# Performance work log

Measured on AMD Instinct MI355X. Metric: run time of the kernel, lower is better.

The kernel has to match this reference:

```python
import jax, jax.numpy as jnp
import numpy as np

# Clebsch-Gordan coefficients in the real basis; l=1 components stored in (y,z,x) order
S2 = 1.0 / np.sqrt(2.0)
S3 = 1.0 / np.sqrt(3.0)
S6 = 1.0 / np.sqrt(6.0)
_C2 = np.zeros((5, 3, 3), np.float32)
_C2[0, 2, 0] = _C2[0, 0, 2] = S2          # ~ xy
_C2[1, 0, 1] = _C2[1, 1, 0] = S2          # ~ yz
_C2[2, 1, 1] = 2.0 * S6                   # ~ 2z^2 - x^2 - y^2
_C2[2, 2, 2] = -S6
_C2[2, 0, 0] = -S6
_C2[3, 2, 1] = _C2[3, 1, 2] = S2          # ~ xz
_C2[4, 2, 2] = S2                          # ~ x^2 - y^2
_C2[4, 0, 0] = -S2
C2 = jnp.asarray(_C2)

N0, N1 = 64, 32        # multiplicities of input 0e / 1o irreps
CUTOFF = 5.0


def basis_functions(pos):
    """pos [N,3] -> (scalars [N,64], l=1 features [N,32,3])."""
    r = jnp.linalg.norm(pos, axis=-1, keepdims=True) + 1e-9        # [N,1]
    d = pos[:, (1, 2, 0)] / r                                       # unit dir, (y,z,x) order
    c0 = jnp.linspace(0.0, CUTOFF, N0, dtype=pos.dtype)
    c1 = jnp.linspace(0.0, CUTOFF, N1, dtype=pos.dtype)
    f0 = jnp.exp(-4.0 * (r - c0) ** 2)                              # [N,64] gaussian RBF
    f1 = jnp.exp(-4.0 * (r - c1) ** 2)                              # [N,32]
    x1 = f1[:, :, None] * d[:, None, :]                             # [N,32,3]
    return f0, x1


def lin_l(x, W):
    # channel mixing within one irrep block; preserves the m axis if present
    if x.ndim == 2:
        return x @ W
    return jnp.einsum('ncm,cd->ndm', x, W)


def tensor_product(a0, a1, b0, b1):
    """Full uvw CG tensor product of (64x0 + 32x1) x (64x0 + 32x1)."""
    N = a0.shape[0]
    # l=0 outputs: 0x0->0 and 1x1->0
    p000 = jnp.einsum('na,nb->nab', a0, b0).reshape(N, -1)                 # [N,4096]
    p110 = jnp.einsum('nam,nbm->nab', a1, b1).reshape(N, -1) * S3          # [N,1024]
    t0 = jnp.concatenate([p000, p110], axis=1)                             # [N,5120]
    # l=1 outputs: 0x1->1, 1x0->1, 1x1->1 (cross product)
    p011 = (a0[:, :, None, None] * b1[:, None, :, :]).reshape(N, -1, 3)    # [N,2048,3]
    p101 = (a1[:, :, None, :] * b0[:, None, :, None]).reshape(N, -1, 3)    # [N,2048,3]
    p111 = (jnp.cross(a1[:, :, None, :], b1[:, None, :, :]) * S2).reshape(N, -1, 3)
    t1 = jnp.concatenate([p011, p101, p111], axis=1)                       # [N,5120,3]
    # l=2 output: 1x1->2 via CG tensor
    t2 = jnp.einsum('nai,nbj,mij->nabm', a1, b1, C2).reshape(N, -1, 5)     # [N,1024,5]
    return t0, t1, t2


def setup_inputs() -> dict:
    key = jax.random.key(0)
    ks = jax.random.split(key, 10)
    N = 4096
    def w(k, i, o):
        return jax.random.normal(k, (i, o), jnp.float32) / np.sqrt(i)
    return {
        'positions': jax.random.normal(ks[0], (N, 3), jnp.float32) * 2.0,
        'W1_0': w(ks[1], 64, 64),
        'W1_1': w(ks[2], 32, 32),
        'W2_0': w(ks[3], 64, 64),
        'W2_1': w(ks[4], 32, 32),
        'W3_0': w(ks[5], 5120, 64),
        'W3_1': w(ks[6], 5120, 32),
        'W3_2': w(ks[7], 1024, 16),
        'W_out': w(ks[8], 240, 7),
        'b_out': jnp.zeros((7,), jnp.float32),
    }


def reference(positions, W1_0, W1_1, W2_0, W2_1, W3_0, W3_1, W3_2, W_out, b_out):
    f0, f1 = basis_functions(positions)                 # 64x0, 32x1
    a0, a1 = lin_l(f0, W1_0), lin_l(f1, W1_1)           # linear1
    b0, b1 = lin_l(f0, W2_0), lin_l(f1, W2_1)           # linear2
    t0, t1, t2 = tensor_product(a0, a1, b0, b1)         # 5120x0, 5120x1, 1024x2
    y0 = lin_l(t0, W3_0)                                # [N,64]
    y1 = lin_l(t1, W3_1)                                # [N,32,3]
    y2 = lin_l(t2, W3_2)                                # [N,16,5]
    N = y0.shape[0]
    feat = jnp.concatenate([y0, y1.reshape(N, -1), y2.reshape(N, -1)], axis=1)  # [N,240]
    return feat @ W_out + b_out                         # [N,7]
```

## Files before the change

### kernel.cpp

```cpp
#include <hip/hip_runtime.h>
#include <math.h>

#define NS2 0.70710678118654752440f
#define NS3 0.57735026918962576451f
#define NS6 0.40824829046386301636f

typedef _Float16 f16;
typedef _Float16 f16x8 __attribute__((ext_vector_type(8)));
typedef float    f32x4 __attribute__((ext_vector_type(4)));

#define GT_K    22528
#define UV_ROW  216
#define OFF_UV  157696

__device__ __forceinline__ void build_gt(
    const float* __restrict__ W3_0, const float* __restrict__ W3_1,
    const float* __restrict__ W3_2, const float* __restrict__ Wout,
    f16* __restrict__ wsh, float* smem, int k_base, int n_k)
{
    const int tid = threadIdx.x;
    float* s_wo  = smem;
    float* s_red = smem + 1680;
    for (int i = tid; i < 1680; i += 256) s_wo[i] = Wout[i];
    __syncthreads();
    const int kl = tid & 63, q = tid >> 6;
    if (kl < n_k) {
        const int k = k_base + kl;
        float acc[7] = {0.f,0.f,0.f,0.f,0.f,0.f,0.f};
        if (k < 4096) {
            const float* wr = W3_0 + (size_t)k * 64;
            #pragma unroll
            for (int oo = 0; oo < 16; oo += 4) {
                int o = q*16 + oo;
                float4 wv = *(const float4*)(wr + o);
                const float* w0 = s_wo + o * 7;
                #pragma unroll
                for (int kk = 0; kk < 7; ++kk)
                    acc[kk] = fmaf(wv.x, w0[kk], fmaf(wv.y, w0[7+kk],
                              fmaf(wv.z, w0[14+kk], fmaf(wv.w, w0[21+kk], acc[kk]))));
            }
        } else if (k < 10240) {
            int it = k >> 6, s = it - 64, m = s >> 5, a2 = s & 31, l = k & 63;
            const float* wr = W3_1 + (size_t)(2048 + a2*64 + l) * 32;
            #pragma unroll
            for (int oo = 0; oo < 8; oo += 4) {
                int o = q*8 + oo;
                float4 wv = *(const float4*)(wr + o);
                const float* w0 = s_wo + (64 + o*3 + m) * 7;
                #pragma unroll
                for (int kk = 0; kk < 7; ++kk)
                    acc[kk] = fmaf(wv.x, w0[kk], fmaf(wv.y, w0[21+kk],
                              fmaf(wv.z, w0[42+kk], fmaf(wv.w, w0[63+kk], acc[kk]))));
            }
        } else {
            int it2 = (k - 10240) >> 5, l32 = k & 31;
            if (it2 < 32) {
                const float* wr = W3_0 + (size_t)(4096 + it2*32 + l32) * 64;
                #pragma unroll
                for (int oo = 0; oo < 16; oo += 4) {
                    int o = q*16 + oo;
                    float4 wv = *(const float4*)(wr + o);
                    const float* w0 = s_wo + o * 7;
                    #pragma unroll
                    for (int kk = 0; kk < 7; ++kk)
                        acc[kk] = fmaf(wv.x, w0[kk], fmaf(wv.y, w0[7+kk],
                                  fmaf(wv.z, w0[14+kk], fmaf(wv.w, w0[21+kk], acc[kk]))));
                }
            } else if (it2 < 224) {
                int t = it2 - 32, m = t >> 6, a = t & 63;
                const float* wr = W3_1 + (size_t)(a*32 + l32) * 32;
                #pragma unroll
                for (int oo = 0; oo < 8; oo += 4) {
                    int o = q*8 + oo;
                    float4 wv = *(const float4*)(wr + o);
                    const float* w0 = s_wo + (64 + o*3 + m) * 7;
                    #pragma unroll
                    for (int kk = 0; kk < 7; ++kk)
                        acc[kk] = fmaf(wv.x, w0[kk], fmaf(wv.y, w0[21+kk],
                                  fmaf(wv.z, w0[42+kk], fmaf(wv.w, w0[63+kk], acc[kk]))));
                }
            } else {
                int t = it2 - 224, m = t >> 5, a = t & 31;
                const float* wr = W3_2 + (size_t)(a*32 + l32) * 16;
                int o = q*4;
                float4 wv = *(const float4*)(wr + o);
                const float* w0 = s_wo + (160 + o*5 + m) * 7;
                #pragma unroll
                for (int kk = 0; kk < 7; ++kk)
                    acc[kk] = fmaf(wv.x, w0[kk], fmaf(wv.y, w0[35+kk],
                              fmaf(wv.z, w0[70+kk], fmaf(wv.w, w0[105+kk], acc[kk]))));
            }
        }
        #pragma unroll
        for (int r = 0; r < 7; ++r) s_red[(q*64 + kl)*8 + r] = acc[r];
    }
    __syncthreads();
    if (tid < n_k) {
        #pragma unroll
        for (int r = 0; r < 7; ++r) {
            float v = s_red[(      tid)*8 + r] + s_red[( 64 + tid)*8 + r]
                    + s_red[(128 + tid)*8 + r] + s_red[(192 + tid)*8 + r];
            wsh[(size_t)r * GT_K + k_base + tid] = (f16)v;
        }
    }
}

__device__ __forceinline__ void build_nodes(
    const float* __restrict__ pos,
    const float* __restrict__ W1_0, const float* __restrict__ W1_1,
    const float* __restrict__ W2_0, const float* __restrict__ W2_1,
    const float* __restrict__ bout,
    f16* __restrict__ wsh, float* __restrict__ out, float* smem, int base)
{
    const int tid = threadIdx.x;
    float* s_f0 = smem;
    float* s_f1 = smem + 512;
    f16* uv = wsh + OFF_UV;
    {
        int d = tid & 63;
        #pragma unroll
        for (int jj = 0; jj < 2; ++jj) {
            int j = (tid >> 6) + jj * 4;
            int n = base + j;
            float px = pos[n*3+0], py = pos[n*3+1], pz = pos[n*3+2];
            float r  = sqrtf(px*px + py*py + pz*pz) + 1e-9f;
            float t0 = r - (5.0f/63.0f) * (float)d;
            s_f0[j*64 + d] = __expf(-4.f * t0 * t0);
        }
        {
            int j = tid >> 5, d1 = tid & 31;
            int n = base + j;
            float px = pos[n*3+0], py = pos[n*3+1], pz = pos[n*3+2];
            float r  = sqrtf(px*px + py*py + pz*pz) + 1e-9f;
            float t1 = r - (5.0f/31.0f) * (float)d1;
            s_f1[j*32 + d1] = __expf(-4.f * t1 * t1);
        }
        if (tid < 8) {
            int n = base + tid;
            float px = pos[n*3+0], py = pos[n*3+1], pz = pos[n*3+2];
            float r  = sqrtf(px*px + py*py + pz*pz) + 1e-9f;
            float iv = 1.0f / r;
            float d0 = py*iv, d1 = pz*iv, d2 = px*iv;
            f16* row = uv + (size_t)n * UV_ROW;
            row[192+0] = (f16)d0;
            row[192+1] = (f16)d1;
            row[192+2] = (f16)d2;
            row[192+3] = (f16)(NS3 * (d0*d0 + d1*d1 + d2*d2));
            row[192+4] = (f16)(2.f*NS2*d2*d0);
            row[192+5] = (f16)(2.f*NS2*d0*d1);
            row[192+6] = (f16)(NS6*(2.f*d1*d1 - d2*d2 - d0*d0));
            row[192+7] = (f16)(2.f*NS2*d2*d1);
            row[192+8] = (f16)(NS2*(d2*d2 - d0*d0));
            row[201]   = (f16)1.0f;
        }
        if (tid < 56) out[base*7 + tid] = bout[tid % 7];
    }
    __syncthreads();
    {
        int c = tid & 63, jb = tid >> 6;
        float aa0 = 0.f, aa1 = 0.f, ba0 = 0.f, ba1 = 0.f;
        const float* wa = W1_0 + c;
        const float* wb = W2_0 + c;
        #pragma unroll 4
        for (int d = 0; d < 64; ++d) {
            float wav = wa[d*64], wbv = wb[d*64];
            float fA = s_f0[jb*64 + d], fB = s_f0[(jb+4)*64 + d];
            aa0 = fmaf(fA, wav, aa0);  aa1 = fmaf(fB, wav, aa1);
            ba0 = fmaf(fA, wbv, ba0);  ba1 = fmaf(fB, wbv, ba1);
        }
        uv[(size_t)(base+jb  )*UV_ROW +      c] = (f16)aa0;
        uv[(size_t)(base+jb+4)*UV_ROW +      c] = (f16)aa1;
        uv[(size_t)(base+jb  )*UV_ROW + 96 + c] = (f16)ba0;
        uv[(size_t)(base+jb+4)*UV_ROW + 96 + c] = (f16)ba1;

        int c1 = tid & 31, j8 = tid >> 5;
        float aA = 0.f, aB = 0.f;
        const float* wA = W1_1 + c1;
        const float* wB = W2_1 + c1;
        #pragma unroll 4
        for (int d = 0; d < 32; ++d) {
            float f = s_f1[j8*32 + d];
            aA = fmaf(f, wA[d*32], aA);
            aB = fmaf(f, wB[d*32], aB);
        }
        uv[(size_t)(base+j8)*UV_ROW +  64 + c1] = (f16)aA;
        uv[(size_t)(base+j8)*UV_ROW + 160 + c1] = (f16)aB;
    }
}

__global__ __launch_bounds__(256) void prep_kernel(
    const float* __restrict__ pos,
    const float* __restrict__ W1_0, const float* __restrict__ W1_1,
    const float* __restrict__ W2_0, const float* __restrict__ W2_1,
    const float* __restrict__ W3_0, const float* __restrict__ W3_1,
    const float* __restrict__ W3_2, const float* __restrict__ Wout,
    const float* __restrict__ bout,
    f16* __restrict__ wsh, float* __restrict__ out, int N)
{
    __shared__ __align__(16) float smem[3728];
    (void)N;
    build_gt(W3_0, W3_1, W3_2, Wout, wsh, smem, blockIdx.x * 44, 44);
    build_nodes(pos, W1_0, W1_1, W2_0, W2_1, bout, wsh, out, smem,
                blockIdx.x * 8);
}

__global__ __launch_bounds__(256) void main_kernel(
    const f16* __restrict__ wsh, float* __restrict__ out, int N)
{
    __shared__ __align__(16) char smem[79248];
    f16* s_g   = (f16*)smem;
    f16* s_uv  = (f16*)(smem + 39648);
    f16* s_ugt = (f16*)(smem + 67296);
    unsigned short* s_idx = (unsigned short*)(smem + 79072);
    (void)N;

    const int tid  = threadIdx.x;
    const int w    = tid >> 6;
    const int lane = tid & 63;
    const int lq   = lane >> 4;
    const int lm   = lane & 15;
    const int ra   = lm % 7;
    const int g    = blockIdx.x >> 3;
    const int kq   = blockIdx.x & 7;

    uint4 ru[7];
    {
        const uint4* src = (const uint4*)(wsh + OFF_UV + (size_t)g * 64 * UV_ROW);
        #pragma unroll
        for (int it = 0; it < 7; ++it) {
            int j = tid + it*256;
            if (j < 1728) ru[it] = src[j];
        }
    }
    uint4 rg[10];
    #pragma unroll
    for (int it = 0; it < 10; ++it) {
        int j = tid + it*256;
        if (j < 2464) {
            int row = j / 352, col = j - row*352;
            size_t off = (size_t)row * GT_K +
                         (col < 160 ? kq*1280 + col*8
                                    : 10240 + kq*1536 + (col-160)*8);
            rg[it] = *(const uint4*)(wsh + off);
        }
    }
    if (tid < 88) {
        int c  = tid;
        int gc = (c < 40) ? (kq*40 + c) : (320 + kq*48 + (c - 40));
        int uidx, gidx;
        if (gc < 320) {
            int it = gc >> 1;
            if (it < 64) { uidx = it; gidx = 9; }
            else { int s = it - 64; uidx = 64 + (s & 31); gidx = s >> 5; }
        } else {
            int it2 = gc - 320;
            if (it2 < 32)       { uidx = 64 + it2;                  gidx = 3; }
            else if (it2 < 224) { int t = it2 - 32;  uidx = t & 63;         gidx = t >> 6; }
            else                { int t = it2 - 224; uidx = 64 + (t & 31);  gidx = 4 + (t >> 5); }
        }
        s_idx[c] = (unsigned short)(uidx | (gidx << 8));
    }
    {
        uint4* dst = (uint4*)s_uv;
        #pragma unroll
        for (int it = 0; it < 7; ++it) {
            int j = tid + it*256;
            if (j < 1728) dst[j] = ru[it];
        }
    }
    #pragma unroll
    for (int it = 0; it < 10; ++it) {
        int j = tid + it*256;
        if (j < 2464) {
            int row = j / 352, col = j - row*352;
            *(uint4*)(s_g + row*2832 + col*8) = rg[it];
        }
    }
    __syncthreads();

    #pragma unroll
    for (int it = 0; it < 22; ++it) {
        int j = tid + it*256;
        int n = j / 88, c = j - n*88;
        unsigned short ix = s_idx[c];
        float u  = (float)s_uv[n*UV_ROW + (ix & 255)];
        float gg = (float)s_uv[n*UV_ROW + 192 + (ix >> 8)];
        s_ugt[n*92 + c] = (f16)(u * gg);
    }
    const f16* myrow = s_uv + (w*16 + lm) * UV_ROW;
    f16x8 vA0 = *(const f16x8*)(myrow +  96 + lq*8);
    f16x8 vA1 = *(const f16x8*)(myrow + 128 + lq*8);
    f16x8 vB  = *(const f16x8*)(myrow + 160 + lq*8);
    __syncthreads();

    f32x4 acc0 = {0.f,0.f,0.f,0.f}, acc1 = {0.f,0.f,0.f,0.f};
    const f16* arow  = s_g + ra*2832 + lq*8;
    const f16* ugrow = s_ugt + (w*16 + lm)*92;
    #pragma unroll
    for (int cb = 0; cb < 5; ++cb) {
        f16x8 ug8 = *(const f16x8*)(ugrow + cb*8);
        #pragma unroll
        for (int s = 0; s < 8; ++s) {
            int c = cb*8 + s;
            f16x8 a  = *(const f16x8*)(arow + c*32);
            f16x8 vv = (s & 1) ? vA1 : vA0;
            f16 ug   = ug8[s];
            f16x8 b;
            #pragma unroll
            for (int j2 = 0; j2 < 8; ++j2) b[j2] = vv[j2] * ug;
            if (s & 1) acc1 = __builtin_amdgcn_mfma_f32_16x16x32_f16(a, b, acc1, 0, 0, 0);
            else       acc0 = __builtin_amdgcn_mfma_f32_16x16x32_f16(a, b, acc0, 0, 0, 0);
        }
    }
    #pragma unroll
    for (int cb = 5; cb < 11; ++cb) {
        f16x8 ug8 = *(const f16x8*)(ugrow + cb*8);
        #pragma unroll
        for (int s = 0; s < 8; ++s) {
            int c = cb*8 + s;
            f16x8 a  = *(const f16x8*)(arow + c*32);
            f16 ug   = ug8[s];
            f16x8 b;
            #pragma unroll
            for (int j2 = 0; j2 < 8; ++j2) b[j2] = vB[j2] * ug;
            if (s & 1) acc1 = __builtin_amdgcn_mfma_f32_16x16x32_f16(a, b, acc1, 0, 0, 0);
            else       acc0 = __builtin_amdgcn_mfma_f32_16x16x32_f16(a, b, acc0, 0, 0, 0);
        }
    }

    int node = g*64 + w*16 + lm;
    if (lq == 0) {
        #pragma unroll
        for (int r = 0; r < 4; ++r) atomicAdd(&out[node*7 + r], acc0[r] + acc1[r]);
    } else if (lq == 1) {
        #pragma unroll
        for (int r = 0; r < 3; ++r) atomicAdd(&out[node*7 + 4 + r], acc0[r] + acc1[r]);
    }
}

extern "C" void kernel_launch(void* const* d_in, const int* in_sizes, int n_in,
                              void* d_out, int out_size, void* d_ws, size_t ws_size,
                              hipStream_t stream)
{
    const float* pos  = (const float*)d_in[0];
    const float* W1_0 = (const float*)d_in[1];
    const float* W1_1 = (const float*)d_in[2];
    const float* W2_0 = (const float*)d_in[3];
    const float* W2_1 = (const float*)d_in[4];
    const float* W3_0 = (const float*)d_in[5];
    const float* W3_1 = (const float*)d_in[6];
    const float* W3_2 = (const float*)d_in[7];
    const float* Wout = (const float*)d_in[8];
    const float* bout = (const float*)d_in[9];
    f16*   wsh = (f16*)d_ws;
    float* op  = (float*)d_out;
    int N = in_sizes[0] / 3;

    prep_kernel<<<512, 256, 0, stream>>>(pos, W1_0, W1_1, W2_0, W2_1,
                                         W3_0, W3_1, W3_2, Wout, bout, wsh, op, N);
    main_kernel<<<512, 256, 0, stream>>>(wsh, op, N);
}
```

Baseline: 104.8 us.

## Move node features into main kernel and double-buffer weight slices over K

Per-node feature construction (RBF, linear1/2, direction harmonics) moves from the prep kernel into the main kernel, so node data stays in shared memory instead of going through global workspace. Each main block now owns 16 nodes and loops over all 8 K-slices of the folded weight matrix. The next slice is loaded into a double buffer while the current one is computed, with K split across waves. Per-wave partial sums are reduced in shared memory and written once with the bias, replacing atomicAdd. The trade-off is fewer blocks (256), roughly 93 KB of shared memory per block with one block per CU, and the weights being re-read by every block.

```diff
diff --git a/kernel.cpp b/kernel.cpp
--- a/kernel.cpp
+++ b/kernel.cpp
@@ -9,26 +9,51 @@
 typedef _Float16 f16x8 __attribute__((ext_vector_type(8)));
 typedef float    f32x4 __attribute__((ext_vector_type(4)));
 
-#define GT_K    22528
-#define UV_ROW  216
-#define OFF_UV  157696
-
-__device__ __forceinline__ void build_gt(
+#define EI 19712
+
+__global__ __launch_bounds__(256) void prep_kernel(
     const float* __restrict__ W3_0, const float* __restrict__ W3_1,
     const float* __restrict__ W3_2, const float* __restrict__ Wout,
-    f16* __restrict__ wsh, float* smem, int k_base, int n_k)
+    f16* __restrict__ wsh)
 {
-    const int tid = threadIdx.x;
+    __shared__ __align__(16) float smem[3728];
     float* s_wo  = smem;
     float* s_red = smem + 1680;
+    const int tid = threadIdx.x;
     for (int i = tid; i < 1680; i += 256) s_wo[i] = Wout[i];
     __syncthreads();
     const int kl = tid & 63, q = tid >> 6;
-    if (kl < n_k) {
-        const int k = k_base + kl;
-        float acc[7] = {0.f,0.f,0.f,0.f,0.f,0.f,0.f};
-        if (k < 4096) {
-            const float* wr = W3_0 + (size_t)k * 64;
+    const int k  = blockIdx.x * 64 + kl;
+    float acc[7] = {0.f,0.f,0.f,0.f,0.f,0.f,0.f};
+    if (k < 4096) {
+        const float* wr = W3_0 + (size_t)k * 64;
+        #pragma unroll
+        for (int oo = 0; oo < 16; oo += 4) {
+            int o = q*16 + oo;
+            float4 wv = *(const float4*)(wr + o);
+            const float* w0 = s_wo + o * 7;
+            #pragma unroll
+            for (int kk = 0; kk < 7; ++kk)
+                acc[kk] = fmaf(wv.x, w0[kk], fmaf(wv.y, w0[7+kk],
+                          fmaf(wv.z, w0[14+kk], fmaf(wv.w, w0[21+kk], acc[kk]))));
+        }
+    } else if (k < 10240) {
+        int it = k >> 6, s = it - 64, m = s >> 5, a2 = s & 31, l = k & 63;
+        const float* wr = W3_1 + (size_t)(2048 + a2*64 + l) * 32;
+        #pragma unroll
+        for (int oo = 0; oo < 8; oo += 4) {
+            int o = q*8 + oo;
+            float4 wv = *(const float4*)(wr + o);
+            const float* w0 = s_wo + (64 + o*3 + m) * 7;
+            #pragma unroll
+            for (int kk = 0; kk < 7; ++kk)
+                acc[kk] = fmaf(wv.x, w0[kk], fmaf(wv.y, w0[21+kk],
+                          fmaf(wv.z, w0[42+kk], fmaf(wv.w, w0[63+kk], acc[kk]))));
+        }
+    } else {
+        int it2 = (k - 10240) >> 5, l32 = k & 31;
+        if (it2 < 32) {
+            const float* wr = W3_0 + (size_t)(4096 + it2*32 + l32) * 64;
             #pragma unroll
             for (int oo = 0; oo < 16; oo += 4) {
                 int o = q*16 + oo;
@@ -39,9 +64,9 @@
                     acc[kk] = fmaf(wv.x, w0[kk], fmaf(wv.y, w0[7+kk],
                               fmaf(wv.z, w0[14+kk], fmaf(wv.w, w0[21+kk], acc[kk]))));
             }
-        } else if (k < 10240) {
-            int it = k >> 6, s = it - 64, m = s >> 5, a2 = s & 31, l = k & 63;
-            const float* wr = W3_1 + (size_t)(2048 + a2*64 + l) * 32;
+        } else if (it2 < 224) {
+            int t = it2 - 32, m = t >> 6, a = t & 63;
+            const float* wr = W3_1 + (size_t)(a*32 + l32) * 32;
             #pragma unroll
             for (int oo = 0; oo < 8; oo += 4) {
                 int o = q*8 + oo;
@@ -53,288 +78,250 @@
                               fmaf(wv.z, w0[42+kk], fmaf(wv.w, w0[63+kk], acc[kk]))));
             }
         } else {
-            int it2 = (k - 10240) >> 5, l32 = k & 31;
-            if (it2 < 32) {
-                const float* wr = W3_0 + (size_t)(4096 + it2*32 + l32) * 64;
-                #pragma unroll
-                for (int oo = 0; oo < 16; oo += 4) {
-                    int o = q*16 + oo;
-                    float4 wv = *(const float4*)(wr + o);
-                    const float* w0 = s_wo + o * 7;
-                    #pragma unroll
-                    for (int kk = 0; kk < 7; ++kk)
-                        acc[kk] = fmaf(wv.x, w0[kk], fmaf(wv.y, w0[7+kk],
-                                  fmaf(wv.z, w0[14+kk], fmaf(wv.w, w0[21+kk], acc[kk]))));
-                }
-            } else if (it2 < 224) {
-                int t = it2 - 32, m = t >> 6, a = t & 63;
-                const float* wr = W3_1 + (size_t)(a*32 + l32) * 32;
-                #pragma unroll
-                for (int oo = 0; oo < 8; oo += 4) {
-                    int o = q*8 + oo;
-                    float4 wv = *(const float4*)(wr + o);
-                    const float* w0 = s_wo + (64 + o*3 + m) * 7;
-                    #pragma unroll
-                    for (int kk = 0; kk < 7; ++kk)
-                        acc[kk] = fmaf(wv.x, w0[kk], fmaf(wv.y, w0[21+kk],
-                                  fmaf(wv.z, w0[42+kk], fmaf(wv.w, w0[63+kk], acc[kk]))));
-                }
-            } else {
-                int t = it2 - 224, m = t >> 5, a = t & 31;
-                const float* wr = W3_2 + (size_t)(a*32 + l32) * 16;
-                int o = q*4;
-                float4 wv = *(const float4*)(wr + o);
-                const float* w0 = s_wo + (160 + o*5 + m) * 7;
-                #pragma unroll
-                for (int kk = 0; kk < 7; ++kk)
-                    acc[kk] = fmaf(wv.x, w0[kk], fmaf(wv.y, w0[35+kk],
-                              fmaf(wv.z, w0[70+kk], fmaf(wv.w, w0[105+kk], acc[kk]))));
-            }
-        }
-        #pragma unroll
-        for (int r = 0; r < 7; ++r) s_red[(q*64 + kl)*8 + r] = acc[r];
-    }
-    __syncthreads();
-    if (tid < n_k) {
+            int t = it2 - 224, m = t >> 5, a = t & 31;
+            const float* wr = W3_2 + (size_t)(a*32 + l32) * 16;
+            int o = q*4;
+            float4 wv = *(const float4*)(wr + o);
+            const float* w0 = s_wo + (160 + o*5 + m) * 7;
+            #pragma unroll
+            for (int kk = 0; kk < 7; ++kk)
+                acc[kk] = fmaf(wv.x, w0[kk], fmaf(wv.y, w0[35+kk],
+                          fmaf(wv.z, w0[70+kk], fmaf(wv.w, w0[105+kk], acc[kk]))));
+        }
+    }
+    #pragma unroll
+    for (int r = 0; r < 7; ++r) s_red[(q*64 + kl)*8 + r] = acc[r];
+    __syncthreads();
+    if (tid < 64) {
+        int kk2 = blockIdx.x * 64 + tid;
+        int e, j;
+        if (kk2 < 10240) { e = kk2 / 1280; j = kk2 - e*1280; }
+        else { int kb = kk2 - 10240; e = kb / 1536; j = 1280 + kb - e*1536; }
+        f16* dst = wsh + e*EI + j;
         #pragma unroll
         for (int r = 0; r < 7; ++r) {
             float v = s_red[(      tid)*8 + r] + s_red[( 64 + tid)*8 + r]
                     + s_red[(128 + tid)*8 + r] + s_red[(192 + tid)*8 + r];
-            wsh[(size_t)r * GT_K + k_base + tid] = (f16)v;
+            dst[r*2816] = (f16)v;
         }
     }
 }
 
-__device__ __forceinline__ void build_nodes(
+__global__ __launch_bounds__(256, 1) void main_kernel(
+    const f16* __restrict__ wsh,
     const float* __restrict__ pos,
     const float* __restrict__ W1_0, const float* __restrict__ W1_1,
     const float* __restrict__ W2_0, const float* __restrict__ W2_1,
     const float* __restrict__ bout,
-    f16* __restrict__ wsh, float* __restrict__ out, float* smem, int base)
+    float* __restrict__ out, int N)
 {
-    const int tid = threadIdx.x;
-    float* s_f0 = smem;
-    float* s_f1 = smem + 512;
-    f16* uv = wsh + OFF_UV;
+    __shared__ __align__(16) char smem[93248];
+    f16* s_g   = (f16*)smem;
+    f16* s_uv  = (f16*)(smem + 79296);
+    f16* s_ugt = (f16*)(smem + 86208);
+    unsigned short* s_idx = (unsigned short*)(smem + 91840);
+    float* s_f0 = (float*)smem;
+    float* s_f1 = (float*)(smem + 4096);
+    (void)N;
+
+    const int tid  = threadIdx.x;
+    const int base = blockIdx.x * 16;
+
     {
         int d = tid & 63;
         #pragma unroll
-        for (int jj = 0; jj < 2; ++jj) {
-            int j = (tid >> 6) + jj * 4;
-            int n = base + j;
-            float px = pos[n*3+0], py = pos[n*3+1], pz = pos[n*3+2];
+        for (int it = 0; it < 4; ++it) {
+            int n = (tid >> 6) + it*4;
+            const float* pp = pos + (size_t)(base + n) * 3;
+            float px = pp[0], py = pp[1], pz = pp[2];
             float r  = sqrtf(px*px + py*py + pz*pz) + 1e-9f;
             float t0 = r - (5.0f/63.0f) * (float)d;
-            s_f0[j*64 + d] = __expf(-4.f * t0 * t0);
-        }
-        {
-            int j = tid >> 5, d1 = tid & 31;
-            int n = base + j;
-            float px = pos[n*3+0], py = pos[n*3+1], pz = pos[n*3+2];
+            s_f0[n*64 + d] = __expf(-4.f * t0 * t0);
+        }
+        int d1 = tid & 31;
+        #pragma unroll
+        for (int it = 0; it < 2; ++it) {
+            int n = (tid >> 5) + it*8;
+            const float* pp = pos + (size_t)(base + n) * 3;
+            float px = pp[0], py = pp[1], pz = pp[2];
             float r  = sqrtf(px*px + py*py + pz*pz) + 1e-9f;
             float t1 = r - (5.0f/31.0f) * (float)d1;
-            s_f1[j*32 + d1] = __expf(-4.f * t1 * t1);
-        }
-        if (tid < 8) {
-            int n = base + tid;
-            float px = pos[n*3+0], py = pos[n*3+1], pz = pos[n*3+2];
+            s_f1[n*32 + d1] = __expf(-4.f * t1 * t1);
+        }
+        if (tid < 16) {
+            const float* pp = pos + (size_t)(base + tid) * 3;
+            float px = pp[0], py = pp[1], pz = pp[2];
             float r  = sqrtf(px*px + py*py + pz*pz) + 1e-9f;
             float iv = 1.0f / r;
-            float d0 = py*iv, d1 = pz*iv, d2 = px*iv;
-            f16* row = uv + (size_t)n * UV_ROW;
+            float d0 = py*iv, dz = pz*iv, dx = px*iv;
+            f16* row = s_uv + tid*216;
             row[192+0] = (f16)d0;
-            row[192+1] = (f16)d1;
-            row[192+2] = (f16)d2;
-            row[192+3] = (f16)(NS3 * (d0*d0 + d1*d1 + d2*d2));
-            row[192+4] = (f16)(2.f*NS2*d2*d0);
-            row[192+5] = (f16)(2.f*NS2*d0*d1);
-            row[192+6] = (f16)(NS6*(2.f*d1*d1 - d2*d2 - d0*d0));
-            row[192+7] = (f16)(2.f*NS2*d2*d1);
-            row[192+8] = (f16)(NS2*(d2*d2 - d0*d0));
+            row[192+1] = (f16)dz;
+            row[192+2] = (f16)dx;
+            row[192+3] = (f16)(NS3 * (d0*d0 + dz*dz + dx*dx));
+            row[192+4] = (f16)(2.f*NS2*dx*d0);
+            row[192+5] = (f16)(2.f*NS2*d0*dz);
+            row[192+6] = (f16)(NS6*(2.f*dz*dz - dx*dx - d0*d0));
+            row[192+7] = (f16)(2.f*NS2*dx*dz);
+            row[192+8] = (f16)(NS2*(dx*dx - d0*d0));
             row[201]   = (f16)1.0f;
         }
-        if (tid < 56) out[base*7 + tid] = bout[tid % 7];
-    }
-    __syncthreads();
+        for (int c = tid; c < 704; c += 256) {
+            int p  = c / 88, cl = c - p*88;
+            int gc = (cl < 40) ? p*40 + cl : 320 + p*48 + (cl - 40);
+            int uidx, gidx;
+            if (gc < 320) {
+                int it = gc >> 1;
+                if (it < 64) { uidx = it; gidx = 9; }
+                else { int s = it - 64; uidx = 64 + (s & 31); gidx = s >> 5; }
+            } else {
+                int it2 = gc - 320;
+                if (it2 < 32)       { uidx = 64 + it2;                  gidx = 3; }
+                else if (it2 < 224) { int t = it2 - 32;  uidx = t & 63;         gidx = t >> 6; }
+                else                { int t = it2 - 224; uidx = 64 + (t & 31);  gidx = 4 + (t >> 5); }
+            }
+            s_idx[c] = (unsigned short)(uidx | (gidx << 8));
+        }
+    }
+    __syncthreads();
+
     {
         int c = tid & 63, jb = tid >> 6;
-        float aa0 = 0.f, aa1 = 0.f, ba0 = 0.f, ba1 = 0.f;
+        float a0a[4] = {0,0,0,0}, b0a[4] = {0,0,0,0};
         const float* wa = W1_0 + c;
         const float* wb = W2_0 + c;
-        #pragma unroll 4
         for (int d = 0; d < 64; ++d) {
             float wav = wa[d*64], wbv = wb[d*64];
-            float fA = s_f0[jb*64 + d], fB = s_f0[(jb+4)*64 + d];
-            aa0 = fmaf(fA, wav, aa0);  aa1 = fmaf(fB, wav, aa1);
-            ba0 = fmaf(fA, wbv, ba0);  ba1 = fmaf(fB, wbv, ba1);
-        }
-        uv[(size_t)(base+jb  )*UV_ROW +      c] = (f16)aa0;
-        uv[(size_t)(base+jb+4)*UV_ROW +      c] = (f16)aa1;
-        uv[(size_t)(base+jb  )*UV_ROW + 96 + c] = (f16)ba0;
-        uv[(size_t)(base+jb+4)*UV_ROW + 96 + c] = (f16)ba1;
-
+            #pragma unroll
+            for (int m = 0; m < 4; ++m) {
+                float f = s_f0[(jb + 4*m)*64 + d];
+                a0a[m] = fmaf(f, wav, a0a[m]);
+                b0a[m] = fmaf(f, wbv, b0a[m]);
+            }
+        }
+        #pragma unroll
+        for (int m = 0; m < 4; ++m) {
+            s_uv[(jb + 4*m)*216 +      c] = (f16)a0a[m];
+            s_uv[(jb + 4*m)*216 + 96 + c] = (f16)b0a[m];
+        }
         int c1 = tid & 31, j8 = tid >> 5;
-        float aA = 0.f, aB = 0.f;
+        float Aa[2] = {0,0}, Ba[2] = {0,0};
         const float* wA = W1_1 + c1;
         const float* wB = W2_1 + c1;
-        #pragma unroll 4
         for (int d = 0; d < 32; ++d) {
-            float f = s_f1[j8*32 + d];
-            aA = fmaf(f, wA[d*32], aA);
-            aB = fmaf(f, wB[d*32], aB);
-        }
-        uv[(size_t)(base+j8)*UV_ROW +  64 + c1] = (f16)aA;
-        uv[(size_t)(base+j8)*UV_ROW + 160 + c1] = (f16)aB;
-    }
-}
-
-__global__ __launch_bounds__(256) void prep_kernel(
-    const float* __restrict__ pos,
-    const float* __restrict__ W1_0, const float* __restrict__ W1_1,
-    const float* __restrict__ W2_0, const float* __restrict__ W2_1,
-    const float* __restrict__ W3_0, const float* __restrict__ W3_1,
-    const float* __restrict__ W3_2, const float* __restrict__ Wout,
-    const float* __restrict__ bout,
-    f16* __restrict__ wsh, float* __restrict__ out, int N)
-{
-    __shared__ __align__(16) float smem[3728];
-    (void)N;
-    build_gt(W3_0, W3_1, W3_2, Wout, wsh, smem, blockIdx.x * 44, 44);
-    build_nodes(pos, W1_0, W1_1, W2_0, W2_1, bout, wsh, out, smem,
-                blockIdx.x * 8);
-}
-
-__global__ __launch_bounds__(256) void main_kernel(
-    const f16* __restrict__ wsh, float* __restrict__ out, int N)
-{
-    __shared__ __align__(16) char smem[79248];
-    f16* s_g   = (f16*)smem;
-    f16* s_uv  = (f16*)(smem + 39648);
-    f16* s_ugt = (f16*)(smem + 67296);
-    unsigned short* s_idx = (unsigned short*)(smem + 79072);
-    (void)N;
-
-    const int tid  = threadIdx.x;
+            float wAv = wA[d*32], wBv = wB[d*32];
+            #pragma unroll
+            for (int m = 0; m < 2; ++m) {
+                float f = s_f1[(j8 + 8*m)*32 + d];
+                Aa[m] = fmaf(f, wAv, Aa[m]);
+                Ba[m] = fmaf(f, wBv, Ba[m]);
+            }
+        }
+        #pragma unroll
+        for (int m = 0; m < 2; ++m) {
+            s_uv[(j8 + 8*m)*216 +  64 + c1] = (f16)Aa[m];
+            s_uv[(j8 + 8*m)*216 + 160 + c1] = (f16)Ba[m];
+        }
+    }
+    __syncthreads();
+
     const int w    = tid >> 6;
     const int lane = tid & 63;
     const int lq   = lane >> 4;
     const int lm   = lane & 15;
     const int ra   = lm % 7;
-    const int g    = blockIdx.x >> 3;
-    const int kq   = blockIdx.x & 7;
-
-    uint4 ru[7];
-    {
-        const uint4* src = (const uint4*)(wsh + OFF_UV + (size_t)g * 64 * UV_ROW);
-        #pragma unroll
-        for (int it = 0; it < 7; ++it) {
-            int j = tid + it*256;
-            if (j < 1728) ru[it] = src[j];
-        }
-    }
-    uint4 rg[10];
-    #pragma unroll
-    for (int it = 0; it < 10; ++it) {
-        int j = tid + it*256;
-        if (j < 2464) {
-            int row = j / 352, col = j - row*352;
-            size_t off = (size_t)row * GT_K +
-                         (col < 160 ? kq*1280 + col*8
-                                    : 10240 + kq*1536 + (col-160)*8);
-            rg[it] = *(const uint4*)(wsh + off);
-        }
-    }
-    if (tid < 88) {
-        int c  = tid;
-        int gc = (c < 40) ? (kq*40 + c) : (320 + kq*48 + (c - 40));
-        int uidx, gidx;
-        if (gc < 320) {
-            int it = gc >> 1;
-            if (it < 64) { uidx = it; gidx = 9; }
-            else { int s = it - 64; uidx = 64 + (s & 31); gidx = s >> 5; }
-        } else {
-            int it2 = gc - 320;
-            if (it2 < 32)       { uidx = 64 + it2;                  gidx = 3; }
-            else if (it2 < 224) { int t = it2 - 32;  uidx = t & 63;         gidx = t >> 6; }
-            else                { int t = it2 - 224; uidx = 64 + (t & 31);  gidx = 4 + (t >> 5); }
-        }
-        s_idx[c] = (unsigned short)(uidx | (gidx << 8));
-    }
-    {
-        uint4* dst = (uint4*)s_uv;
-        #pragma unroll
-        for (int it = 0; it < 7; ++it) {
-            int j = tid + it*256;
-            if (j < 1728) dst[j] = ru[it];
-        }
-    }
-    #pragma unroll
-    for (int it = 0; it < 10; ++it) {
-        int j = tid + it*256;
-        if (j < 2464) {
-            int row = j / 352, col = j - row*352;
-            *(uint4*)(s_g + row*2832 + col*8) = rg[it];
-        }
-    }
-    __syncthreads();
-
-    #pragma unroll
-    for (int it = 0; it < 22; ++it) {
-        int j = tid + it*256;
-        int n = j / 88, c = j - n*88;
-        unsigned short ix = s_idx[c];
-        float u  = (float)s_uv[n*UV_ROW + (ix & 255)];
-        float gg = (float)s_uv[n*UV_ROW + 192 + (ix >> 8)];
-        s_ugt[n*92 + c] = (f16)(u * gg);
-    }
-    const f16* myrow = s_uv + (w*16 + lm) * UV_ROW;
+    const f16* myrow = s_uv + lm*216;
     f16x8 vA0 = *(const f16x8*)(myrow +  96 + lq*8);
     f16x8 vA1 = *(const f16x8*)(myrow + 128 + lq*8);
     f16x8 vB  = *(const f16x8*)(myrow + 160 + lq*8);
-    __syncthreads();
+
+    uint4 rg[10];
+    auto stage_load = [&](int p) {
+        const uint4* src = (const uint4*)(wsh + p*EI);
+        #pragma unroll
+        for (int it = 0; it < 10; ++it) {
+            int j = tid + it*256;
+            if (j < 2464) rg[it] = src[j];
+        }
+    };
+    auto stage_write = [&](int buf) {
+        f16* dst0 = s_g + buf*19824;
+        #pragma unroll
+        for (int it = 0; it < 10; ++it) {
+            int j = tid + it*256;
+            if (j < 2464) {
+                int row = j / 352, col = j - row*352;
+                *(uint4*)(dst0 + row*2832 + col*8) = rg[it];
+            }
+        }
+    };
+    auto do_ugt = [&](int p, int buf) {
+        f16* dstu = s_ugt + buf*1408;
+        #pragma unroll
+        for (int it = 0; it < 6; ++it) {
+            int j = tid + it*256;
+            if (j < 1408) {
+                int cl = j >> 4, n = j & 15;
+                unsigned short ix = s_idx[p*88 + cl];
+                float u  = (float)s_uv[n*216 + (ix & 255)];
+                float gg = (float)s_uv[n*216 + 192 + (ix >> 8)];
+                dstu[cl*16 + n] = (f16)(u * gg);
+            }
+        }
+    };
 
     f32x4 acc0 = {0.f,0.f,0.f,0.f}, acc1 = {0.f,0.f,0.f,0.f};
-    const f16* arow  = s_g + ra*2832 + lq*8;
-    const f16* ugrow = s_ugt + (w*16 + lm)*92;
-    #pragma unroll
-    for (int cb = 0; cb < 5; ++cb) {
-        f16x8 ug8 = *(const f16x8*)(ugrow + cb*8);
-        #pragma unroll
-        for (int s = 0; s < 8; ++s) {
-            int c = cb*8 + s;
-            f16x8 a  = *(const f16x8*)(arow + c*32);
-            f16x8 vv = (s & 1) ? vA1 : vA0;
-            f16 ug   = ug8[s];
+    auto compute = [&](int buf) {
+        const f16* gb = s_g + buf*19824 + ra*2832 + lq*8;
+        const f16* ub = s_ugt + buf*1408;
+        #pragma unroll
+        for (int i = 0; i < 10; ++i) {
+            int c = w*10 + i;
+            f16 ug  = ub[c*16 + lm];
+            f16x8 a = *(const f16x8*)(gb + c*32);
+            f16x8 vv = (i & 1) ? vA1 : vA0;
             f16x8 b;
             #pragma unroll
             for (int j2 = 0; j2 < 8; ++j2) b[j2] = vv[j2] * ug;
-            if (s & 1) acc1 = __builtin_amdgcn_mfma_f32_16x16x32_f16(a, b, acc1, 0, 0, 0);
+            if (i & 1) acc1 = __builtin_amdgcn_mfma_f32_16x16x32_f16(a, b, acc1, 0, 0, 0);
             else       acc0 = __builtin_amdgcn_mfma_f32_16x16x32_f16(a, b, acc0, 0, 0, 0);
         }
-    }
-    #pragma unroll
-    for (int cb = 5; cb < 11; ++cb) {
-        f16x8 ug8 = *(const f16x8*)(ugrow + cb*8);
-        #pragma unroll
-        for (int s = 0; s < 8; ++s) {
-            int c = cb*8 + s;
-            f16x8 a  = *(const f16x8*)(arow + c*32);
-            f16 ug   = ug8[s];
+        #pragma unroll
+        for (int i = 0; i < 12; ++i) {
+            int c = 40 + w*12 + i;
+            f16 ug  = ub[c*16 + lm];
+            f16x8 a = *(const f16x8*)(gb + c*32);
             f16x8 b;
             #pragma unroll
             for (int j2 = 0; j2 < 8; ++j2) b[j2] = vB[j2] * ug;
-            if (s & 1) acc1 = __builtin_amdgcn_mfma_f32_16x16x32_f16(a, b, acc1, 0, 0, 0);
+            if (i & 1) acc1 = __builtin_amdgcn_mfma_f32_16x16x32_f16(a, b, acc1, 0, 0, 0);
             else       acc0 = __builtin_amdgcn_mfma_f32_16x16x32_f16(a, b, acc0, 0, 0, 0);
         }
-    }
-
-    int node = g*64 + w*16 + lm;
-    if (lq == 0) {
-        #pragma unroll
-        for (int r = 0; r < 4; ++r) atomicAdd(&out[node*7 + r], acc0[r] + acc1[r]);
-    } else if (lq == 1) {
-        #pragma unroll
-        for (int r = 0; r < 3; ++r) atomicAdd(&out[node*7 + 4 + r], acc0[r] + acc1[r]);
+    };
+
+    stage_load(0); stage_write(0); do_ugt(0, 0);
+    __syncthreads();
+    for (int p = 0; p < 8; ++p) {
+        int buf = p & 1;
+        if (p < 7) { stage_load(p + 1); do_ugt(p + 1, buf ^ 1); }
+        compute(buf);
+        if (p < 7) stage_write(buf ^ 1);
+        __syncthreads();
+    }
+
+    float* s_part = (float*)smem;
+    if (lq < 2) {
+        int nr = (lq == 0) ? 4 : 3;
+        for (int r = 0; r < nr; ++r)
+            s_part[(w*16 + lm)*8 + lq*4 + r] = acc0[r] + acc1[r];
+    }
+    __syncthreads();
+    if (tid < 112) {
+        int n = tid / 7, r = tid - n*7;
+        float v = bout[r];
+        #pragma unroll
+        for (int ww = 0; ww < 4; ++ww) v += s_part[(ww*16 + n)*8 + r];
+        out[(size_t)(base + n)*7 + r] = v;
     }
 }
 
@@ -356,7 +343,7 @@
     float* op  = (float*)d_out;
     int N = in_sizes[0] / 3;
 
-    prep_kernel<<<512, 256, 0, stream>>>(pos, W1_0, W1_1, W2_0, W2_1,
-                                         W3_0, W3_1, W3_2, Wout, bout, wsh, op, N);
-    main_kernel<<<512, 256, 0, stream>>>(wsh, op, N);
+    prep_kernel<<<352, 256, 0, stream>>>(W3_0, W3_1, W3_2, Wout, wsh);
+    main_kernel<<<256, 256, 0, stream>>>(wsh, pos, W1_0, W1_1, W2_0, W2_1,
+                                         bout, op, N);
 }
```

New measurement: 127.9 us. +22.0%, slower.
